# Optimization experiments

Measured on AMD Instinct MI355X. Metric: run time of the kernel, lower is better.

## Reference

```python
import jax, jax.numpy as jnp
import numpy as np

N_NODES = 100000
N_EDGES = 3200000
N_FEAT = 128
N_GRAPHS = 256


def setup_inputs() -> dict:
    key = jax.random.key(0)
    ks = jax.random.split(key, 12)
    x = jax.random.normal(ks[0], (N_NODES, N_FEAT), dtype=jnp.float32)
    edge_index = jax.random.randint(ks[1], (2, N_EDGES), 0, N_NODES, dtype=jnp.int64)
    edge_weight = jax.random.uniform(ks[2], (N_EDGES,), dtype=jnp.float32)
    batch = jnp.sort(jax.random.randint(ks[3], (N_NODES,), 0, N_GRAPHS, dtype=jnp.int64))
    def glorot(k, shape):
        lim = np.sqrt(6.0 / (shape[0] + shape[1]))
        return jax.random.uniform(k, shape, dtype=jnp.float32, minval=-lim, maxval=lim)
    W1 = glorot(ks[4], (N_FEAT, 64))
    b1 = jnp.zeros((64,), dtype=jnp.float32)
    W2 = glorot(ks[5], (64, 32))
    b2 = jnp.zeros((32,), dtype=jnp.float32)
    Wl1 = glorot(ks[6], (32, 16))
    bl1 = jnp.zeros((16,), dtype=jnp.float32)
    Wl2 = glorot(ks[7], (16, 1))
    bl2 = jnp.zeros((1,), dtype=jnp.float32)
    return {"x": x, "edge_index": edge_index, "edge_weight": edge_weight,
            "batch": batch, "W1": W1, "b1": b1, "W2": W2, "b2": b2,
            "Wl1": Wl1, "bl1": bl1, "Wl2": Wl2, "bl2": bl2}


def gcn_conv(x, row, col, ew, W, b, num_nodes):
    # x' = D^-1/2 (A + I) D^-1/2 (x W) + b, weights on edges, self-loop weight 1
    h = x @ W  # [N, out]
    deg = jax.ops.segment_sum(ew, col, num_segments=num_nodes) + 1.0  # self-loops add 1
    dinv = jnp.where(deg > 0, jax.lax.rsqrt(deg), 0.0)
    norm = dinv[row] * ew * dinv[col]  # [E]
    msg = h[row] * norm[:, None]  # edge-wise gather + scale
    agg = jax.ops.segment_sum(msg, col, num_segments=num_nodes)
    agg = agg + h * (dinv * dinv)[:, None]  # self-loop contribution
    return agg + b


def reference(x, edge_index, edge_weight, batch, W1, b1, W2, b2, Wl1, bl1, Wl2, bl2):
    row, col = edge_index[0], edge_index[1]
    h = jax.nn.relu(gcn_conv(x, row, col, edge_weight, W1, b1, N_NODES))
    # dropout is identity in eval mode
    h = gcn_conv(h, row, col, edge_weight, W2, b2, N_NODES)
    u = jax.ops.segment_sum(h, batch, num_segments=N_GRAPHS)  # global_add_pool
    out = jax.nn.relu(u @ Wl1 + bl1)
    out = out @ Wl2 + bl2
    return out.reshape(-1)
```

## Files before the change

kernel.cpp:

```cpp
#include <hip/hip_runtime.h>
#include <hip/hip_bf16.h>

#define N_NODES 100000
#define N_EDGES 3200000
#define N_GRAPHS 256

#define NBUCK 391
#define SORT_ITEMS 4096
#define NB_SORT ((N_EDGES + SORT_ITEMS - 1) / SORT_ITEMS)
#define HIST_N (NBUCK * NB_SORT)
#define ROW_MASK 131071

__device__ __forceinline__ float bfl(int d) {
    return __uint_as_float(((unsigned)d) << 16);
}
__device__ __forceinline__ float bfh(int d) {
    return __uint_as_float(((unsigned)d) & 0xffff0000u);
}
__device__ __forceinline__ unsigned short f2bf(float f) {
    __hip_bfloat16 b = __float2bfloat16(f);
    return *(unsigned short*)&b;
}

__global__ __launch_bounds__(256) void hist_kernel(const int* __restrict__ col,
                                                   int* __restrict__ hist) {
    __shared__ int h[NBUCK];
    int tid = threadIdx.x;
    for (int i = tid; i < NBUCK; i += 256) h[i] = 0;
    __syncthreads();
    int base = blockIdx.x * SORT_ITEMS + tid * 4;
    #pragma unroll
    for (int l = 0; l < SORT_ITEMS / 1024; ++l) {
        int e = base + l * 1024;
        if (e < N_EDGES) {
            int4 c4 = *(const int4*)&col[e];
            atomicAdd(&h[c4.x >> 8], 1);
            atomicAdd(&h[c4.y >> 8], 1);
            atomicAdd(&h[c4.z >> 8], 1);
            atomicAdd(&h[c4.w >> 8], 1);
        }
    }
    __syncthreads();
    for (int i = tid; i < NBUCK; i += 256) hist[i * NB_SORT + blockIdx.x] = h[i];
}

__global__ __launch_bounds__(256) void scanA_kernel(int* __restrict__ a,
                                                    int* __restrict__ bsum, int n) {
    __shared__ int s[256];
    int tid = threadIdx.x;
    int base = blockIdx.x * 4096 + tid * 16;
    int v[16];
    int sum = 0;
    #pragma unroll
    for (int i = 0; i < 16; ++i) { v[i] = (base + i < n) ? a[base + i] : 0; sum += v[i]; }
    s[tid] = sum;
    __syncthreads();
    for (int d = 1; d < 256; d <<= 1) {
        int x = (tid >= d) ? s[tid - d] : 0;
        __syncthreads();
        s[tid] += x;
        __syncthreads();
    }
    int run = s[tid] - sum;
    #pragma unroll
    for (int i = 0; i < 16; ++i) {
        if (base + i < n) a[base + i] = run;
        run += v[i];
    }
    if (tid == 255) bsum[blockIdx.x] = s[255];
}

__global__ __launch_bounds__(256) void scanB_kernel(int* bsum, int nb) {
    __shared__ int s[256];
    int tid = threadIdx.x;
    int v = (tid < nb) ? bsum[tid] : 0;
    s[tid] = v;
    __syncthreads();
    for (int d = 1; d < 256; d <<= 1) {
        int x = (tid >= d) ? s[tid - d] : 0;
        __syncthreads();
        s[tid] += x;
        __syncthreads();
    }
    if (tid < nb) bsum[tid] = s[tid] - v;
}

__global__ __launch_bounds__(256) void scanC_kernel(int* a, const int* __restrict__ bsum, int n) {
    int i = blockIdx.x * 256 + threadIdx.x;
    if (i < n) a[i] += bsum[i >> 12];
}

__global__ __launch_bounds__(256) void scatter_sort_kernel(const int* __restrict__ col,
                                                           const int* __restrict__ row,
                                                           const float* __restrict__ ew,
                                                           const int* __restrict__ hist,
                                                           int2* __restrict__ rw2) {
    __shared__ int offs[NBUCK];
    int tid = threadIdx.x;
    for (int i = tid; i < NBUCK; i += 256) offs[i] = hist[i * NB_SORT + blockIdx.x];
    __syncthreads();
    int base = blockIdx.x * SORT_ITEMS + tid * 4;
    #pragma unroll
    for (int l = 0; l < SORT_ITEMS / 1024; ++l) {
        int e = base + l * 1024;
        if (e < N_EDGES) {
            int4 c4 = *(const int4*)&col[e];
            int4 r4 = *(const int4*)&row[e];
            float4 w4 = *(const float4*)&ew[e];
            int p0 = atomicAdd(&offs[c4.x >> 8], 1);
            int p1 = atomicAdd(&offs[c4.y >> 8], 1);
            int p2 = atomicAdd(&offs[c4.z >> 8], 1);
            int p3 = atomicAdd(&offs[c4.w >> 8], 1);
            int2 v0; v0.x = r4.x | ((c4.x & 255) << 17); v0.y = __float_as_int(w4.x);
            int2 v1; v1.x = r4.y | ((c4.y & 255) << 17); v1.y = __float_as_int(w4.y);
            int2 v2; v2.x = r4.z | ((c4.z & 255) << 17); v2.y = __float_as_int(w4.z);
            int2 v3; v3.x = r4.w | ((c4.w & 255) << 17); v3.y = __float_as_int(w4.w);
            rw2[p0] = v0;
            rw2[p1] = v1;
            rw2[p2] = v2;
            rw2[p3] = v3;
        }
    }
}

__global__ __launch_bounds__(256) void build_kernel(const int* __restrict__ hist,
                                                    const int2* __restrict__ rw2,
                                                    int* __restrict__ off,
                                                    int* __restrict__ cnt,
                                                    float* __restrict__ dinv,
                                                    int2* __restrict__ csr) {
    int b = blockIdx.x;
    int tid = threadIdx.x;
    int begin = hist[b * NB_SORT];
    int end = (b + 1 < NBUCK) ? hist[(b + 1) * NB_SORT] : N_EDGES;
    __shared__ int lcnt[256];
    __shared__ float ldeg[256];
    __shared__ int s[256];
    __shared__ int curo[256];
    lcnt[tid] = 0;
    ldeg[tid] = 0.f;
    __syncthreads();
    for (int e = begin + tid; e < end; e += 1024) {
        int2 a0 = rw2[e];
        int e1 = e + 256, e2 = e + 512, e3 = e + 768;
        int2 a1 = (e1 < end) ? rw2[e1] : make_int2(0, 0);
        int2 a2 = (e2 < end) ? rw2[e2] : make_int2(0, 0);
        int2 a3 = (e3 < end) ? rw2[e3] : make_int2(0, 0);
        atomicAdd(&lcnt[a0.x >> 17], 1);
        atomicAdd(&ldeg[a0.x >> 17], __int_as_float(a0.y));
        if (e1 < end) { atomicAdd(&lcnt[a1.x >> 17], 1); atomicAdd(&ldeg[a1.x >> 17], __int_as_float(a1.y)); }
        if (e2 < end) { atomicAdd(&lcnt[a2.x >> 17], 1); atomicAdd(&ldeg[a2.x >> 17], __int_as_float(a2.y)); }
        if (e3 < end) { atomicAdd(&lcnt[a3.x >> 17], 1); atomicAdd(&ldeg[a3.x >> 17], __int_as_float(a3.y)); }
    }
    __syncthreads();
    int v = lcnt[tid];
    s[tid] = v;
    __syncthreads();
    for (int d = 1; d < 256; d <<= 1) {
        int x = (tid >= d) ? s[tid - d] : 0;
        __syncthreads();
        s[tid] += x;
        __syncthreads();
    }
    int excl = s[tid] - v;
    int node = (b << 8) + tid;
    if (node < N_NODES) {
        off[node] = begin + excl;
        cnt[node] = v;
        dinv[node] = rsqrtf(1.0f + ldeg[tid]);
    }
    curo[tid] = begin + excl;
    __syncthreads();
    for (int e = begin + tid; e < end; e += 1024) {
        int2 a0 = rw2[e];
        int e1 = e + 256, e2 = e + 512, e3 = e + 768;
        int2 a1 = (e1 < end) ? rw2[e1] : make_int2(0, 0);
        int2 a2 = (e2 < end) ? rw2[e2] : make_int2(0, 0);
        int2 a3 = (e3 < end) ? rw2[e3] : make_int2(0, 0);
        int p0 = atomicAdd(&curo[a0.x >> 17], 1);
        csr[p0] = make_int2(a0.x & ROW_MASK, a0.y);
        if (e1 < end) { int p = atomicAdd(&curo[a1.x >> 17], 1); csr[p] = make_int2(a1.x & ROW_MASK, a1.y); }
        if (e2 < end) { int p = atomicAdd(&curo[a2.x >> 17], 1); csr[p] = make_int2(a2.x & ROW_MASK, a2.y); }
        if (e3 < end) { int p = atomicAdd(&curo[a3.x >> 17], 1); csr[p] = make_int2(a3.x & ROW_MASK, a3.y); }
    }
}

template <int IN, int OUT, int ROWS>
__global__ __launch_bounds__(256) void gemm_bf16_kernel(const float* __restrict__ X,
                                                        const float* __restrict__ W,
                                                        const float* __restrict__ scale,
                                                        unsigned short* __restrict__ H, int n) {
    constexpr int BK = 16;
    constexpr int TX = OUT / 4;
    constexpr int TY = ROWS / 8;
    static_assert(TX * TY == 256, "block must be 256 threads");
    __shared__ float xsT[BK][ROWS + 4];
    __shared__ float ws[BK][OUT + 4];
    int tid = threadIdx.x;
    int tx = tid % TX, ty = tid / TX;
    int r0 = blockIdx.x * ROWS;
    float acc[8][4] = {};
    for (int k0 = 0; k0 < IN; k0 += BK) {
        constexpr int XL = (ROWS * BK) / (256 * 4);
        #pragma unroll
        for (int l = 0; l < XL; ++l) {
            int t = tid + l * 256;
            int rr = t >> 2;
            int kp = (t & 3) * 4;
            float4 v = make_float4(0.f, 0.f, 0.f, 0.f);
            int gr = r0 + rr;
            if (gr < n) v = *(const float4*)&X[(size_t)gr * IN + k0 + kp];
            xsT[kp + 0][rr] = v.x;
            xsT[kp + 1][rr] = v.y;
            xsT[kp + 2][rr] = v.z;
            xsT[kp + 3][rr] = v.w;
        }
        constexpr int WL = (BK * OUT) / 4;
        if (WL == 256 || tid < WL) {
            int kr = tid / TX;
            int cp = (tid % TX) * 4;
            float4 v = *(const float4*)&W[(size_t)(k0 + kr) * OUT + cp];
            *(float4*)&ws[kr][cp] = v;
        }
        __syncthreads();
        #pragma unroll
        for (int kk = 0; kk < BK; ++kk) {
            float4 a0 = *(const float4*)&xsT[kk][ty * 8];
            float4 a1 = *(const float4*)&xsT[kk][ty * 8 + 4];
            float4 b = *(const float4*)&ws[kk][tx * 4];
            float av[8] = {a0.x, a0.y, a0.z, a0.w, a1.x, a1.y, a1.z, a1.w};
            float bv[4] = {b.x, b.y, b.z, b.w};
            #pragma unroll
            for (int i = 0; i < 8; ++i) {
                #pragma unroll
                for (int j = 0; j < 4; ++j) acc[i][j] = fmaf(av[i], bv[j], acc[i][j]);
            }
        }
        __syncthreads();
    }
    #pragma unroll
    for (int i = 0; i < 8; ++i) {
        int gr = r0 + ty * 8 + i;
        if (gr < n) {
            float sc = scale[gr];
            ushort4 o;
            o.x = f2bf(acc[i][0] * sc);
            o.y = f2bf(acc[i][1] * sc);
            o.z = f2bf(acc[i][2] * sc);
            o.w = f2bf(acc[i][3] * sc);
            *(ushort4*)&H[(size_t)gr * OUT + tx * 4] = o;
        }
    }
}

__global__ __launch_bounds__(256) void agg1_kernel(const int2* __restrict__ csr,
                                                   const int* __restrict__ off,
                                                   const int* __restrict__ cnt,
                                                   const float* __restrict__ dinv,
                                                   const unsigned short* __restrict__ h1t,
                                                   const float* __restrict__ b1,
                                                   float* __restrict__ h1p) {
    int lane = threadIdx.x & 63;
    int node = blockIdx.x * 4 + (threadIdx.x >> 6);
    int es = lane >> 3;
    int fb = lane & 7;
    int s = off[node], c = cnt[node];
    float acc[8] = {};
    for (int j0 = 0; j0 < c; j0 += 64) {
        int m = min(64, c - j0);
        int2 e = make_int2(0, 0);
        if (lane < m) e = csr[s + j0 + lane];
        int ng = (m + 7) >> 3;
        int g = 0;
        for (; g + 2 <= ng; g += 2) {
            int s0 = g * 8 + es;
            int s1 = s0 + 8;
            int r0 = __shfl(e.x, s0);
            float w0 = __int_as_float(__shfl(e.y, s0));
            int r1 = __shfl(e.x, s1);
            float w1 = __int_as_float(__shfl(e.y, s1));
            int4 d0 = *(const int4*)(h1t + (((size_t)r0) << 6) + (fb << 3));
            int4 d1 = *(const int4*)(h1t + (((size_t)r1) << 6) + (fb << 3));
            acc[0] = fmaf(w0, bfl(d0.x), acc[0]);
            acc[1] = fmaf(w0, bfh(d0.x), acc[1]);
            acc[2] = fmaf(w0, bfl(d0.y), acc[2]);
            acc[3] = fmaf(w0, bfh(d0.y), acc[3]);
            acc[4] = fmaf(w0, bfl(d0.z), acc[4]);
            acc[5] = fmaf(w0, bfh(d0.z), acc[5]);
            acc[6] = fmaf(w0, bfl(d0.w), acc[6]);
            acc[7] = fmaf(w0, bfh(d0.w), acc[7]);
            acc[0] = fmaf(w1, bfl(d1.x), acc[0]);
            acc[1] = fmaf(w1, bfh(d1.x), acc[1]);
            acc[2] = fmaf(w1, bfl(d1.y), acc[2]);
            acc[3] = fmaf(w1, bfh(d1.y), acc[3]);
            acc[4] = fmaf(w1, bfl(d1.z), acc[4]);
            acc[5] = fmaf(w1, bfh(d1.z), acc[5]);
            acc[6] = fmaf(w1, bfl(d1.w), acc[6]);
            acc[7] = fmaf(w1, bfh(d1.w), acc[7]);
        }
        if (g < ng) {
            int s0 = g * 8 + es;
            int r0 = __shfl(e.x, s0);
            float w0 = __int_as_float(__shfl(e.y, s0));
            int4 d0 = *(const int4*)(h1t + (((size_t)r0) << 6) + (fb << 3));
            acc[0] = fmaf(w0, bfl(d0.x), acc[0]);
            acc[1] = fmaf(w0, bfh(d0.x), acc[1]);
            acc[2] = fmaf(w0, bfl(d0.y), acc[2]);
            acc[3] = fmaf(w0, bfh(d0.y), acc[3]);
            acc[4] = fmaf(w0, bfl(d0.z), acc[4]);
            acc[5] = fmaf(w0, bfh(d0.z), acc[5]);
            acc[6] = fmaf(w0, bfl(d0.w), acc[6]);
            acc[7] = fmaf(w0, bfh(d0.w), acc[7]);
        }
    }
    #pragma unroll
    for (int mask = 8; mask <= 32; mask <<= 1) {
        #pragma unroll
        for (int k = 0; k < 8; ++k) acc[k] += __shfl_xor(acc[k], mask);
    }
    if (es == 0) {
        float di = dinv[node];
        int4 ds = *(const int4*)(h1t + (((size_t)node) << 6) + (fb << 3));
        float4 bv0 = *(const float4*)&b1[fb * 8];
        float4 bv1 = *(const float4*)&b1[fb * 8 + 4];
        float4 o0, o1;
        o0.x = fmaxf(fmaf(acc[0] + bfl(ds.x), di, bv0.x), 0.f);
        o0.y = fmaxf(fmaf(acc[1] + bfh(ds.x), di, bv0.y), 0.f);
        o0.z = fmaxf(fmaf(acc[2] + bfl(ds.y), di, bv0.z), 0.f);
        o0.w = fmaxf(fmaf(acc[3] + bfh(ds.y), di, bv0.w), 0.f);
        o1.x = fmaxf(fmaf(acc[4] + bfl(ds.z), di, bv1.x), 0.f);
        o1.y = fmaxf(fmaf(acc[5] + bfh(ds.z), di, bv1.y), 0.f);
        o1.z = fmaxf(fmaf(acc[6] + bfl(ds.w), di, bv1.z), 0.f);
        o1.w = fmaxf(fmaf(acc[7] + bfh(ds.w), di, bv1.w), 0.f);
        float* po = h1p + (size_t)node * 64 + fb * 8;
        *(float4*)po = o0;
        *(float4*)(po + 4) = o1;
    }
}

__global__ __launch_bounds__(256) void agg2_kernel(const int2* __restrict__ csr,
                                                   const int* __restrict__ off,
                                                   const int* __restrict__ cnt,
                                                   const float* __restrict__ dinv,
                                                   const unsigned short* __restrict__ h2t,
                                                   const float* __restrict__ b2,
                                                   float* __restrict__ h2p) {
    int lane = threadIdx.x & 63;
    int half = lane >> 5;
    int hl = lane & 31;
    int es = hl >> 2;
    int fb = hl & 3;
    int wid = threadIdx.x >> 6;
    int node = blockIdx.x * 8 + wid * 2 + half;
    int s = off[node], c = cnt[node];
    int lbase = half << 5;
    float acc[8] = {};
    for (int j0 = 0; j0 < c; j0 += 32) {
        int m = min(32, c - j0);
        int2 e = make_int2(0, 0);
        if (hl < m) e = csr[s + j0 + hl];
        int ng = (m + 7) >> 3;
        int g = 0;
        for (; g + 2 <= ng; g += 2) {
            int s0 = lbase + g * 8 + es;
            int s1 = s0 + 8;
            int r0 = __shfl(e.x, s0);
            float w0 = __int_as_float(__shfl(e.y, s0));
            int r1 = __shfl(e.x, s1);
            float w1 = __int_as_float(__shfl(e.y, s1));
            int4 d0 = *(const int4*)(h2t + (((size_t)r0) << 5) + (fb << 3));
            int4 d1 = *(const int4*)(h2t + (((size_t)r1) << 5) + (fb << 3));
            acc[0] = fmaf(w0, bfl(d0.x), acc[0]);
            acc[1] = fmaf(w0, bfh(d0.x), acc[1]);
            acc[2] = fmaf(w0, bfl(d0.y), acc[2]);
            acc[3] = fmaf(w0, bfh(d0.y), acc[3]);
            acc[4] = fmaf(w0, bfl(d0.z), acc[4]);
            acc[5] = fmaf(w0, bfh(d0.z), acc[5]);
            acc[6] = fmaf(w0, bfl(d0.w), acc[6]);
            acc[7] = fmaf(w0, bfh(d0.w), acc[7]);
            acc[0] = fmaf(w1, bfl(d1.x), acc[0]);
            acc[1] = fmaf(w1, bfh(d1.x), acc[1]);
            acc[2] = fmaf(w1, bfl(d1.y), acc[2]);
            acc[3] = fmaf(w1, bfh(d1.y), acc[3]);
            acc[4] = fmaf(w1, bfl(d1.z), acc[4]);
            acc[5] = fmaf(w1, bfh(d1.z), acc[5]);
            acc[6] = fmaf(w1, bfl(d1.w), acc[6]);
            acc[7] = fmaf(w1, bfh(d1.w), acc[7]);
        }
        if (g < ng) {
            int s0 = lbase + g * 8 + es;
            int r0 = __shfl(e.x, s0);
            float w0 = __int_as_float(__shfl(e.y, s0));
            int4 d0 = *(const int4*)(h2t + (((size_t)r0) << 5) + (fb << 3));
            acc[0] = fmaf(w0, bfl(d0.x), acc[0]);
            acc[1] = fmaf(w0, bfh(d0.x), acc[1]);
            acc[2] = fmaf(w0, bfl(d0.y), acc[2]);
            acc[3] = fmaf(w0, bfh(d0.y), acc[3]);
            acc[4] = fmaf(w0, bfl(d0.z), acc[4]);
            acc[5] = fmaf(w0, bfh(d0.z), acc[5]);
            acc[6] = fmaf(w0, bfl(d0.w), acc[6]);
            acc[7] = fmaf(w0, bfh(d0.w), acc[7]);
        }
    }
    #pragma unroll
    for (int mask = 4; mask <= 16; mask <<= 1) {
        #pragma unroll
        for (int k = 0; k < 8; ++k) acc[k] += __shfl_xor(acc[k], mask);
    }
    if (es == 0) {
        float di = dinv[node];
        int4 ds = *(const int4*)(h2t + (((size_t)node) << 5) + (fb << 3));
        float4 bv0 = *(const float4*)&b2[fb * 8];
        float4 bv1 = *(const float4*)&b2[fb * 8 + 4];
        float4 o0, o1;
        o0.x = fmaf(acc[0] + bfl(ds.x), di, bv0.x);
        o0.y = fmaf(acc[1] + bfh(ds.x), di, bv0.y);
        o0.z = fmaf(acc[2] + bfl(ds.y), di, bv0.z);
        o0.w = fmaf(acc[3] + bfh(ds.y), di, bv0.w);
        o1.x = fmaf(acc[4] + bfl(ds.z), di, bv1.x);
        o1.y = fmaf(acc[5] + bfh(ds.z), di, bv1.y);
        o1.z = fmaf(acc[6] + bfl(ds.w), di, bv1.z);
        o1.w = fmaf(acc[7] + bfh(ds.w), di, bv1.w);
        float* po = h2p + (size_t)node * 32 + fb * 8;
        *(float4*)po = o0;
        *(float4*)(po + 4) = o1;
    }
}

__global__ __launch_bounds__(256) void pool_kernel(const float* __restrict__ h2p,
                                                   const int* __restrict__ batch,
                                                   float* __restrict__ u) {
    int g = blockIdx.x;
    int lo = 0, hi = N_NODES;
    while (lo < hi) { int m = (lo + hi) >> 1; if (batch[m] < g) lo = m + 1; else hi = m; }
    int start = lo;
    hi = N_NODES;
    while (lo < hi) { int m = (lo + hi) >> 1; if (batch[m] < g + 1) lo = m + 1; else hi = m; }
    int end = lo;
    int f = threadIdx.x & 31, grp = threadIdx.x >> 5;
    float acc = 0.f;
    for (int n = start + grp; n < end; n += 8) acc += h2p[(size_t)n * 32 + f];
    __shared__ float red[8][32];
    red[grp][f] = acc;
    __syncthreads();
    if (threadIdx.x < 32) {
        float sum = 0.f;
        #pragma unroll
        for (int k = 0; k < 8; ++k) sum += red[k][threadIdx.x];
        u[g * 32 + threadIdx.x] = sum;
    }
}

__global__ __launch_bounds__(256) void head_kernel(const float* __restrict__ u,
                                                   const float* __restrict__ Wl1,
                                                   const float* __restrict__ bl1,
                                                   const float* __restrict__ Wl2,
                                                   const float* __restrict__ bl2,
                                                   float* __restrict__ out) {
    int g = threadIdx.x;
    float uu[32];
    #pragma unroll
    for (int k = 0; k < 32; ++k) uu[k] = u[g * 32 + k];
    float o = bl2[0];
    #pragma unroll
    for (int j = 0; j < 16; ++j) {
        float h = bl1[j];
        #pragma unroll
        for (int k = 0; k < 32; ++k) h = fmaf(uu[k], Wl1[k * 16 + j], h);
        o = fmaf(fmaxf(h, 0.f), Wl2[j], o);
    }
    out[g] = o;
}

extern "C" void kernel_launch(void* const* d_in, const int* in_sizes, int n_in,
                              void* d_out, int out_size, void* d_ws, size_t ws_size,
                              hipStream_t stream) {
    const float* x     = (const float*)d_in[0];
    const int*   ei    = (const int*)d_in[1];
    const float* ew    = (const float*)d_in[2];
    const int*   batch = (const int*)d_in[3];
    const float* W1    = (const float*)d_in[4];
    const float* b1    = (const float*)d_in[5];
    const float* W2    = (const float*)d_in[6];
    const float* b2    = (const float*)d_in[7];
    const float* Wl1   = (const float*)d_in[8];
    const float* bl1   = (const float*)d_in[9];
    const float* Wl2   = (const float*)d_in[10];
    const float* bl2   = (const float*)d_in[11];
    float* out = (float*)d_out;

    const int* row = ei;
    const int* col = ei + N_EDGES;

    char* p = (char*)d_ws;
    auto alloc = [&](size_t bytes) {
        char* q = p;
        p += (bytes + 255) & ~(size_t)255;
        return q;
    };
    int*   hist   = (int*)alloc((size_t)HIST_N * 4);
    int*   bsum   = (int*)alloc(1024 * 4);
    int2*  rw2    = (int2*)alloc((size_t)N_EDGES * 8);
    int*   off    = (int*)alloc(N_NODES * 4);
    int*   cnt    = (int*)alloc(N_NODES * 4);
    float* dinv   = (float*)alloc(N_NODES * 4);
    int2*  csr    = (int2*)alloc((size_t)N_EDGES * 8);
    unsigned short* h1t = (unsigned short*)rw2;
    float* h1p    = (float*)alloc((size_t)N_NODES * 64 * 4);
    unsigned short* h2t = (unsigned short*)alloc((size_t)N_NODES * 32 * 2);
    float* h2p    = (float*)alloc((size_t)N_NODES * 32 * 4);
    float* u      = (float*)alloc(N_GRAPHS * 32 * 4);

    const int nbScan = (HIST_N + 4095) / 4096;

    hist_kernel<<<NB_SORT, 256, 0, stream>>>(col, hist);
    scanA_kernel<<<nbScan, 256, 0, stream>>>(hist, bsum, HIST_N);
    scanB_kernel<<<1, 256, 0, stream>>>(bsum, nbScan);
    scanC_kernel<<<(HIST_N + 255) / 256, 256, 0, stream>>>(hist, bsum, HIST_N);
    scatter_sort_kernel<<<NB_SORT, 256, 0, stream>>>(col, row, ew, hist, rw2);
    build_kernel<<<NBUCK, 256, 0, stream>>>(hist, rw2, off, cnt, dinv, csr);

    gemm_bf16_kernel<128, 64, 128><<<(N_NODES + 127) / 128, 256, 0, stream>>>(x, W1, dinv, h1t, N_NODES);
    agg1_kernel<<<N_NODES / 4, 256, 0, stream>>>(csr, off, cnt, dinv, h1t, b1, h1p);
    gemm_bf16_kernel<64, 32, 256><<<(N_NODES + 255) / 256, 256, 0, stream>>>(h1p, W2, dinv, h2t, N_NODES);
    agg2_kernel<<<N_NODES / 8, 256, 0, stream>>>(csr, off, cnt, dinv, h2t, b2, h2p);
    pool_kernel<<<N_GRAPHS, 256, 0, stream>>>(h2p, batch, u);
    head_kernel<<<1, 256, 0, stream>>>(u, Wl1, bl1, Wl2, bl2, out);
}
```

Before: 256.1 us.

## Rework CSR build with per-block local sort and global bucket atomics

Replaces the per-block histogram and three-kernel scan with a global bucket-total histogram, a single-block scan, and atomic reservation of per-block ranges. The scatter kernel now sorts each block's edges in shared memory and writes them out contiguously, which is meant to make the global writes coalesced. The build kernel stages each 128-node bucket in shared memory. Buckets longer than the fixed shared-memory capacity fall back to global memory. The agg1 inner loop is also unrolled from 2 to 4 gathers, giving more memory-level parallelism. In exchange, the order of edges within a bucket becomes nondeterministic, and the larger shared-memory footprint may reduce occupancy.

```diff
diff --git a/kernel.cpp b/kernel.cpp
--- a/kernel.cpp
+++ b/kernel.cpp
@@ -5,11 +5,11 @@
 #define N_EDGES 3200000
 #define N_GRAPHS 256
 
-#define NBUCK 391
-#define SORT_ITEMS 4096
+#define NBUCK 782
+#define SORT_ITEMS 8192
 #define NB_SORT ((N_EDGES + SORT_ITEMS - 1) / SORT_ITEMS)
-#define HIST_N (NBUCK * NB_SORT)
 #define ROW_MASK 131071
+#define BCAP 4608
 
 __device__ __forceinline__ float bfl(int d) {
     return __uint_as_float(((unsigned)d) << 16);
@@ -23,7 +23,7 @@
 }
 
 __global__ __launch_bounds__(256) void hist_kernel(const int* __restrict__ col,
-                                                   int* __restrict__ hist) {
+                                                   int* __restrict__ btot) {
     __shared__ int h[NBUCK];
     int tid = threadIdx.x;
     for (int i = tid; i < NBUCK; i += 256) h[i] = 0;
@@ -34,25 +34,30 @@
         int e = base + l * 1024;
         if (e < N_EDGES) {
             int4 c4 = *(const int4*)&col[e];
-            atomicAdd(&h[c4.x >> 8], 1);
-            atomicAdd(&h[c4.y >> 8], 1);
-            atomicAdd(&h[c4.z >> 8], 1);
-            atomicAdd(&h[c4.w >> 8], 1);
-        }
-    }
-    __syncthreads();
-    for (int i = tid; i < NBUCK; i += 256) hist[i * NB_SORT + blockIdx.x] = h[i];
-}
-
-__global__ __launch_bounds__(256) void scanA_kernel(int* __restrict__ a,
-                                                    int* __restrict__ bsum, int n) {
+            atomicAdd(&h[c4.x >> 7], 1);
+            atomicAdd(&h[c4.y >> 7], 1);
+            atomicAdd(&h[c4.z >> 7], 1);
+            atomicAdd(&h[c4.w >> 7], 1);
+        }
+    }
+    __syncthreads();
+    for (int i = tid; i < NBUCK; i += 256) {
+        int c = h[i];
+        if (c) atomicAdd(&btot[i], c);
+    }
+}
+
+__global__ __launch_bounds__(256) void scan_buckets_kernel(const int* __restrict__ btot,
+                                                           int* __restrict__ bstart,
+                                                           int* __restrict__ gcur) {
     __shared__ int s[256];
     int tid = threadIdx.x;
-    int base = blockIdx.x * 4096 + tid * 16;
-    int v[16];
-    int sum = 0;
-    #pragma unroll
-    for (int i = 0; i < 16; ++i) { v[i] = (base + i < n) ? a[base + i] : 0; sum += v[i]; }
+    int i0 = tid * 4;
+    int c0 = (i0 + 0 < NBUCK) ? btot[i0 + 0] : 0;
+    int c1 = (i0 + 1 < NBUCK) ? btot[i0 + 1] : 0;
+    int c2 = (i0 + 2 < NBUCK) ? btot[i0 + 2] : 0;
+    int c3 = (i0 + 3 < NBUCK) ? btot[i0 + 3] : 0;
+    int sum = c0 + c1 + c2 + c3;
     s[tid] = sum;
     __syncthreads();
     for (int d = 1; d < 256; d <<= 1) {
@@ -61,45 +66,67 @@
         s[tid] += x;
         __syncthreads();
     }
-    int run = s[tid] - sum;
-    #pragma unroll
-    for (int i = 0; i < 16; ++i) {
-        if (base + i < n) a[base + i] = run;
-        run += v[i];
-    }
-    if (tid == 255) bsum[blockIdx.x] = s[255];
-}
-
-__global__ __launch_bounds__(256) void scanB_kernel(int* bsum, int nb) {
-    __shared__ int s[256];
-    int tid = threadIdx.x;
-    int v = (tid < nb) ? bsum[tid] : 0;
-    s[tid] = v;
-    __syncthreads();
-    for (int d = 1; d < 256; d <<= 1) {
-        int x = (tid >= d) ? s[tid - d] : 0;
-        __syncthreads();
-        s[tid] += x;
-        __syncthreads();
-    }
-    if (tid < nb) bsum[tid] = s[tid] - v;
-}
-
-__global__ __launch_bounds__(256) void scanC_kernel(int* a, const int* __restrict__ bsum, int n) {
-    int i = blockIdx.x * 256 + threadIdx.x;
-    if (i < n) a[i] += bsum[i >> 12];
+    int excl = s[tid] - sum;
+    if (i0 + 0 < NBUCK) { bstart[i0 + 0] = excl;              gcur[i0 + 0] = excl; }
+    if (i0 + 1 < NBUCK) { bstart[i0 + 1] = excl + c0;         gcur[i0 + 1] = excl + c0; }
+    if (i0 + 2 < NBUCK) { bstart[i0 + 2] = excl + c0 + c1;    gcur[i0 + 2] = excl + c0 + c1; }
+    if (i0 + 3 < NBUCK) { bstart[i0 + 3] = excl + c0 + c1 + c2; gcur[i0 + 3] = excl + c0 + c1 + c2; }
+    if (tid == 255) bstart[NBUCK] = N_EDGES;
 }
 
 __global__ __launch_bounds__(256) void scatter_sort_kernel(const int* __restrict__ col,
                                                            const int* __restrict__ row,
                                                            const float* __restrict__ ew,
-                                                           const int* __restrict__ hist,
+                                                           int* __restrict__ gcur,
                                                            int2* __restrict__ rw2) {
-    __shared__ int offs[NBUCK];
+    __shared__ int lcnt[NBUCK];
+    __shared__ int lofs[NBUCK];
+    __shared__ int lcur[NBUCK];
+    __shared__ int gbase[NBUCK];
+    __shared__ int ps[256];
+    __shared__ int2 buf[SORT_ITEMS];
     int tid = threadIdx.x;
-    for (int i = tid; i < NBUCK; i += 256) offs[i] = hist[i * NB_SORT + blockIdx.x];
+    for (int i = tid; i < NBUCK; i += 256) lcnt[i] = 0;
     __syncthreads();
     int base = blockIdx.x * SORT_ITEMS + tid * 4;
+    #pragma unroll
+    for (int l = 0; l < SORT_ITEMS / 1024; ++l) {
+        int e = base + l * 1024;
+        if (e < N_EDGES) {
+            int4 c4 = *(const int4*)&col[e];
+            atomicAdd(&lcnt[c4.x >> 7], 1);
+            atomicAdd(&lcnt[c4.y >> 7], 1);
+            atomicAdd(&lcnt[c4.z >> 7], 1);
+            atomicAdd(&lcnt[c4.w >> 7], 1);
+        }
+    }
+    __syncthreads();
+    int i0 = tid * 4;
+    int c0 = (i0 + 0 < NBUCK) ? lcnt[i0 + 0] : 0;
+    int c1 = (i0 + 1 < NBUCK) ? lcnt[i0 + 1] : 0;
+    int c2 = (i0 + 2 < NBUCK) ? lcnt[i0 + 2] : 0;
+    int c3 = (i0 + 3 < NBUCK) ? lcnt[i0 + 3] : 0;
+    int sum = c0 + c1 + c2 + c3;
+    ps[tid] = sum;
+    __syncthreads();
+    for (int d = 1; d < 256; d <<= 1) {
+        int x = (tid >= d) ? ps[tid - d] : 0;
+        __syncthreads();
+        ps[tid] += x;
+        __syncthreads();
+    }
+    int excl = ps[tid] - sum;
+    if (i0 + 0 < NBUCK) lofs[i0 + 0] = excl;
+    if (i0 + 1 < NBUCK) lofs[i0 + 1] = excl + c0;
+    if (i0 + 2 < NBUCK) lofs[i0 + 2] = excl + c0 + c1;
+    if (i0 + 3 < NBUCK) lofs[i0 + 3] = excl + c0 + c1 + c2;
+    __syncthreads();
+    for (int i = tid; i < NBUCK; i += 256) {
+        int c = lcnt[i];
+        gbase[i] = c ? atomicAdd(&gcur[i], c) : 0;
+        lcur[i] = lofs[i];
+    }
+    __syncthreads();
     #pragma unroll
     for (int l = 0; l < SORT_ITEMS / 1024; ++l) {
         int e = base + l * 1024;
@@ -107,23 +134,27 @@
             int4 c4 = *(const int4*)&col[e];
             int4 r4 = *(const int4*)&row[e];
             float4 w4 = *(const float4*)&ew[e];
-            int p0 = atomicAdd(&offs[c4.x >> 8], 1);
-            int p1 = atomicAdd(&offs[c4.y >> 8], 1);
-            int p2 = atomicAdd(&offs[c4.z >> 8], 1);
-            int p3 = atomicAdd(&offs[c4.w >> 8], 1);
-            int2 v0; v0.x = r4.x | ((c4.x & 255) << 17); v0.y = __float_as_int(w4.x);
-            int2 v1; v1.x = r4.y | ((c4.y & 255) << 17); v1.y = __float_as_int(w4.y);
-            int2 v2; v2.x = r4.z | ((c4.z & 255) << 17); v2.y = __float_as_int(w4.z);
-            int2 v3; v3.x = r4.w | ((c4.w & 255) << 17); v3.y = __float_as_int(w4.w);
-            rw2[p0] = v0;
-            rw2[p1] = v1;
-            rw2[p2] = v2;
-            rw2[p3] = v3;
-        }
-    }
-}
-
-__global__ __launch_bounds__(256) void build_kernel(const int* __restrict__ hist,
+            int p0 = atomicAdd(&lcur[c4.x >> 7], 1);
+            int p1 = atomicAdd(&lcur[c4.y >> 7], 1);
+            int p2 = atomicAdd(&lcur[c4.z >> 7], 1);
+            int p3 = atomicAdd(&lcur[c4.w >> 7], 1);
+            buf[p0] = make_int2(r4.x | ((c4.x & 127) << 17), __float_as_int(w4.x));
+            buf[p1] = make_int2(r4.y | ((c4.y & 127) << 17), __float_as_int(w4.y));
+            buf[p2] = make_int2(r4.z | ((c4.z & 127) << 17), __float_as_int(w4.z));
+            buf[p3] = make_int2(r4.w | ((c4.w & 127) << 17), __float_as_int(w4.w));
+        }
+    }
+    __syncthreads();
+    int total = min(SORT_ITEMS, N_EDGES - blockIdx.x * SORT_ITEMS);
+    for (int i = tid; i < total; i += 256) {
+        int lo = 0, hi = NBUCK - 1;
+        while (lo < hi) { int mid = (lo + hi + 1) >> 1; if (lofs[mid] <= i) lo = mid; else hi = mid - 1; }
+        int dst = gbase[lo] + (i - lofs[lo]);
+        rw2[dst] = buf[i];
+    }
+}
+
+__global__ __launch_bounds__(256) void build_kernel(const int* __restrict__ bstart,
                                                     const int2* __restrict__ rw2,
                                                     int* __restrict__ off,
                                                     int* __restrict__ cnt,
@@ -131,58 +162,67 @@
                                                     int2* __restrict__ csr) {
     int b = blockIdx.x;
     int tid = threadIdx.x;
-    int begin = hist[b * NB_SORT];
-    int end = (b + 1 < NBUCK) ? hist[(b + 1) * NB_SORT] : N_EDGES;
-    __shared__ int lcnt[256];
-    __shared__ float ldeg[256];
+    int begin = bstart[b];
+    int end = bstart[b + 1];
+    int len = end - begin;
+    __shared__ int2 ebuf[BCAP];
+    __shared__ int2 obuf[BCAP];
+    __shared__ int lcnt[128];
+    __shared__ float ldeg[128];
     __shared__ int s[256];
-    __shared__ int curo[256];
-    lcnt[tid] = 0;
-    ldeg[tid] = 0.f;
-    __syncthreads();
-    for (int e = begin + tid; e < end; e += 1024) {
-        int2 a0 = rw2[e];
-        int e1 = e + 256, e2 = e + 512, e3 = e + 768;
-        int2 a1 = (e1 < end) ? rw2[e1] : make_int2(0, 0);
-        int2 a2 = (e2 < end) ? rw2[e2] : make_int2(0, 0);
-        int2 a3 = (e3 < end) ? rw2[e3] : make_int2(0, 0);
-        atomicAdd(&lcnt[a0.x >> 17], 1);
-        atomicAdd(&ldeg[a0.x >> 17], __int_as_float(a0.y));
-        if (e1 < end) { atomicAdd(&lcnt[a1.x >> 17], 1); atomicAdd(&ldeg[a1.x >> 17], __int_as_float(a1.y)); }
-        if (e2 < end) { atomicAdd(&lcnt[a2.x >> 17], 1); atomicAdd(&ldeg[a2.x >> 17], __int_as_float(a2.y)); }
-        if (e3 < end) { atomicAdd(&lcnt[a3.x >> 17], 1); atomicAdd(&ldeg[a3.x >> 17], __int_as_float(a3.y)); }
-    }
-    __syncthreads();
-    int v = lcnt[tid];
+    __shared__ int curo[128];
+    if (tid < 128) { lcnt[tid] = 0; ldeg[tid] = 0.f; }
+    __syncthreads();
+    for (int i = tid; i < len; i += 1024) {
+        #pragma unroll
+        for (int u = 0; u < 4; ++u) {
+            int ii = i + u * 256;
+            if (ii < len) {
+                int2 a = rw2[begin + ii];
+                if (ii < BCAP) ebuf[ii] = a;
+                int loc = a.x >> 17;
+                atomicAdd(&lcnt[loc], 1);
+                atomicAdd(&ldeg[loc], __int_as_float(a.y));
+            }
+        }
+    }
+    __syncthreads();
+    int v = (tid < 128) ? lcnt[tid] : 0;
     s[tid] = v;
     __syncthreads();
-    for (int d = 1; d < 256; d <<= 1) {
-        int x = (tid >= d) ? s[tid - d] : 0;
-        __syncthreads();
-        s[tid] += x;
-        __syncthreads();
-    }
-    int excl = s[tid] - v;
-    int node = (b << 8) + tid;
-    if (node < N_NODES) {
-        off[node] = begin + excl;
-        cnt[node] = v;
-        dinv[node] = rsqrtf(1.0f + ldeg[tid]);
-    }
-    curo[tid] = begin + excl;
-    __syncthreads();
-    for (int e = begin + tid; e < end; e += 1024) {
-        int2 a0 = rw2[e];
-        int e1 = e + 256, e2 = e + 512, e3 = e + 768;
-        int2 a1 = (e1 < end) ? rw2[e1] : make_int2(0, 0);
-        int2 a2 = (e2 < end) ? rw2[e2] : make_int2(0, 0);
-        int2 a3 = (e3 < end) ? rw2[e3] : make_int2(0, 0);
-        int p0 = atomicAdd(&curo[a0.x >> 17], 1);
-        csr[p0] = make_int2(a0.x & ROW_MASK, a0.y);
-        if (e1 < end) { int p = atomicAdd(&curo[a1.x >> 17], 1); csr[p] = make_int2(a1.x & ROW_MASK, a1.y); }
-        if (e2 < end) { int p = atomicAdd(&curo[a2.x >> 17], 1); csr[p] = make_int2(a2.x & ROW_MASK, a2.y); }
-        if (e3 < end) { int p = atomicAdd(&curo[a3.x >> 17], 1); csr[p] = make_int2(a3.x & ROW_MASK, a3.y); }
-    }
+    for (int d = 1; d < 128; d <<= 1) {
+        int x = (tid >= d && tid < 128) ? s[tid - d] : 0;
+        __syncthreads();
+        if (tid < 128) s[tid] += x;
+        __syncthreads();
+    }
+    if (tid < 128) {
+        int excl = s[tid] - v;
+        int node = (b << 7) + tid;
+        if (node < N_NODES) {
+            off[node] = begin + excl;
+            cnt[node] = v;
+            dinv[node] = rsqrtf(1.0f + ldeg[tid]);
+        }
+        curo[tid] = excl;
+    }
+    __syncthreads();
+    for (int i = tid; i < len; i += 1024) {
+        #pragma unroll
+        for (int u = 0; u < 4; ++u) {
+            int ii = i + u * 256;
+            if (ii < len) {
+                int2 a = (ii < BCAP) ? ebuf[ii] : rw2[begin + ii];
+                int loc = a.x >> 17;
+                int p = atomicAdd(&curo[loc], 1);
+                int2 w = make_int2(a.x & ROW_MASK, a.y);
+                if (p < BCAP) obuf[p] = w; else csr[begin + p] = w;
+            }
+        }
+    }
+    __syncthreads();
+    int lim = min(len, BCAP);
+    for (int i = tid; i < lim; i += 256) csr[begin + i] = obuf[i];
 }
 
 template <int IN, int OUT, int ROWS>
@@ -272,15 +312,20 @@
         if (lane < m) e = csr[s + j0 + lane];
         int ng = (m + 7) >> 3;
         int g = 0;
-        for (; g + 2 <= ng; g += 2) {
+        for (; g + 4 <= ng; g += 4) {
             int s0 = g * 8 + es;
-            int s1 = s0 + 8;
             int r0 = __shfl(e.x, s0);
             float w0 = __int_as_float(__shfl(e.y, s0));
-            int r1 = __shfl(e.x, s1);
-            float w1 = __int_as_float(__shfl(e.y, s1));
+            int r1 = __shfl(e.x, s0 + 8);
+            float w1 = __int_as_float(__shfl(e.y, s0 + 8));
+            int r2 = __shfl(e.x, s0 + 16);
+            float w2 = __int_as_float(__shfl(e.y, s0 + 16));
+            int r3 = __shfl(e.x, s0 + 24);
+            float w3 = __int_as_float(__shfl(e.y, s0 + 24));
             int4 d0 = *(const int4*)(h1t + (((size_t)r0) << 6) + (fb << 3));
             int4 d1 = *(const int4*)(h1t + (((size_t)r1) << 6) + (fb << 3));
+            int4 d2 = *(const int4*)(h1t + (((size_t)r2) << 6) + (fb << 3));
+            int4 d3 = *(const int4*)(h1t + (((size_t)r3) << 6) + (fb << 3));
             acc[0] = fmaf(w0, bfl(d0.x), acc[0]);
             acc[1] = fmaf(w0, bfh(d0.x), acc[1]);
             acc[2] = fmaf(w0, bfl(d0.y), acc[2]);
@@ -297,8 +342,24 @@
             acc[5] = fmaf(w1, bfh(d1.z), acc[5]);
             acc[6] = fmaf(w1, bfl(d1.w), acc[6]);
             acc[7] = fmaf(w1, bfh(d1.w), acc[7]);
-        }
-        if (g < ng) {
+            acc[0] = fmaf(w2, bfl(d2.x), acc[0]);
+            acc[1] = fmaf(w2, bfh(d2.x), acc[1]);
+            acc[2] = fmaf(w2, bfl(d2.y), acc[2]);
+            acc[3] = fmaf(w2, bfh(d2.y), acc[3]);
+            acc[4] = fmaf(w2, bfl(d2.z), acc[4]);
+            acc[5] = fmaf(w2, bfh(d2.z), acc[5]);
+            acc[6] = fmaf(w2, bfl(d2.w), acc[6]);
+            acc[7] = fmaf(w2, bfh(d2.w), acc[7]);
+            acc[0] = fmaf(w3, bfl(d3.x), acc[0]);
+            acc[1] = fmaf(w3, bfh(d3.x), acc[1]);
+            acc[2] = fmaf(w3, bfl(d3.y), acc[2]);
+            acc[3] = fmaf(w3, bfh(d3.y), acc[3]);
+            acc[4] = fmaf(w3, bfl(d3.z), acc[4]);
+            acc[5] = fmaf(w3, bfh(d3.z), acc[5]);
+            acc[6] = fmaf(w3, bfl(d3.w), acc[6]);
+            acc[7] = fmaf(w3, bfh(d3.w), acc[7]);
+        }
+        for (; g < ng; ++g) {
             int s0 = g * 8 + es;
             int r0 = __shfl(e.x, s0);
             float w0 = __int_as_float(__shfl(e.y, s0));
@@ -498,8 +559,9 @@
         p += (bytes + 255) & ~(size_t)255;
         return q;
     };
-    int*   hist   = (int*)alloc((size_t)HIST_N * 4);
-    int*   bsum   = (int*)alloc(1024 * 4);
+    int*   btot   = (int*)alloc(NBUCK * 4);
+    int*   bstart = (int*)alloc((NBUCK + 1) * 4);
+    int*   gcur   = (int*)alloc(NBUCK * 4);
     int2*  rw2    = (int2*)alloc((size_t)N_EDGES * 8);
     int*   off    = (int*)alloc(N_NODES * 4);
     int*   cnt    = (int*)alloc(N_NODES * 4);
@@ -511,14 +573,11 @@
     float* h2p    = (float*)alloc((size_t)N_NODES * 32 * 4);
     float* u      = (float*)alloc(N_GRAPHS * 32 * 4);
 
-    const int nbScan = (HIST_N + 4095) / 4096;
-
-    hist_kernel<<<NB_SORT, 256, 0, stream>>>(col, hist);
-    scanA_kernel<<<nbScan, 256, 0, stream>>>(hist, bsum, HIST_N);
-    scanB_kernel<<<1, 256, 0, stream>>>(bsum, nbScan);
-    scanC_kernel<<<(HIST_N + 255) / 256, 256, 0, stream>>>(hist, bsum, HIST_N);
-    scatter_sort_kernel<<<NB_SORT, 256, 0, stream>>>(col, row, ew, hist, rw2);
-    build_kernel<<<NBUCK, 256, 0, stream>>>(hist, rw2, off, cnt, dinv, csr);
+    hipMemsetAsync(btot, 0, NBUCK * 4, stream);
+    hist_kernel<<<NB_SORT, 256, 0, stream>>>(col, btot);
+    scan_buckets_kernel<<<1, 256, 0, stream>>>(btot, bstart, gcur);
+    scatter_sort_kernel<<<NB_SORT, 256, 0, stream>>>(col, row, ew, gcur, rw2);
+    build_kernel<<<NBUCK, 256, 0, stream>>>(bstart, rw2, off, cnt, dinv, csr);
 
     gemm_bf16_kernel<128, 64, 128><<<(N_NODES + 127) / 128, 256, 0, stream>>>(x, W1, dinv, h1t, N_NODES);
     agg1_kernel<<<N_NODES / 4, 256, 0, stream>>>(csr, off, cnt, dinv, h1t, b1, h1p);
```

After: 269.2 us. +5.1%, slower.
